# Kernel optimization log

Measured on AMD Instinct MI355X. Metric: run time of the kernel, lower is better.

## Reference

```python
import jax, jax.numpy as jnp
import numpy as np

N_EMBD = 768
N_HEAD = 12
HEAD_DIM = N_EMBD // N_HEAD  # 64


def setup_inputs() -> dict:
    key = jax.random.key(0)
    k1, k2, k3 = jax.random.split(key, 3)
    B, S = 4, 2048
    x = jax.random.normal(k1, (B, S, N_EMBD), dtype=jnp.float32)
    W_attn = jax.random.normal(k2, (N_EMBD, 3 * N_EMBD), dtype=jnp.float32) * 0.02
    b_attn = jax.random.normal(k3, (3 * N_EMBD,), dtype=jnp.float32) * 0.02
    return {"x": x, "W_attn": W_attn, "b_attn": b_attn}


def reference(x, W_attn, b_attn):
    B, S, E = x.shape
    H, D = N_HEAD, HEAD_DIM
    # fused QKV projection (torch Linear: x @ W^T + b; here W_attn stored as [E, 3E])
    qkv = x @ W_attn + b_attn  # [B, S, 3E]
    q, k, v = jnp.split(qkv, 3, axis=-1)
    q = q.reshape(B, S, H, D)
    k = k.reshape(B, S, H, D)
    v = v.reshape(B, S, H, D)
    scale = 1.0 / np.sqrt(D).astype(np.float32)
    scores = jnp.einsum('bqhd,bkhd->bhqk', q, k) * scale  # [B, H, S, S]
    causal = jnp.tril(jnp.ones((S, S), dtype=bool))
    # ReLU attention nonlinearity (no softmax); masked entries -> 0
    att = jnp.where(causal, jnp.maximum(scores, 0.0), 0.0)
    y = jnp.einsum('bhqk,bkhd->bqhd', att, v)  # [B, S, H, D]
    return y.reshape(B, S, E)
```

## Files before the change

### kernel.cpp

```cpp
#include <hip/hip_runtime.h>

typedef __attribute__((ext_vector_type(8))) short short8;
typedef __attribute__((ext_vector_type(4))) float floatx4;
typedef __attribute__((ext_vector_type(4))) unsigned int uint4v;

#define S_LEN 2048
#define NH 12
#define HD 64
#define EMB 768
#define E3 2304

#define MF(a, b, c) __builtin_amdgcn_mfma_f32_16x16x32_bf16(a, b, c, 0, 0, 0)

__device__ __forceinline__ unsigned short f2bf(float f) {
    unsigned int u = __builtin_bit_cast(unsigned int, f);
    u += 0x7FFFu + ((u >> 16) & 1u);
    return (unsigned short)(u >> 16);
}

__device__ __forceinline__ unsigned int pack2bf(float a, float b) {
#if __has_builtin(__builtin_amdgcn_cvt_pk_bf16_f32)
    typedef __attribute__((ext_vector_type(2))) short short2v;
    short2v r = __builtin_amdgcn_cvt_pk_bf16_f32(a, b);
    return __builtin_bit_cast(unsigned int, r);
#else
    return (unsigned int)f2bf(a) | ((unsigned int)f2bf(b) << 16);
#endif
}

__device__ __forceinline__ void pl32_swap(unsigned int& x, unsigned int& y) {
#if __has_builtin(__builtin_amdgcn_permlane32_swap)
    typedef __attribute__((ext_vector_type(2))) unsigned int uint2v_;
    uint2v_ r = __builtin_amdgcn_permlane32_swap(x, y, false, false);
    x = r[0]; y = r[1];
#else
    asm("v_permlane32_swap_b32 %0, %1" : "+v"(x), "+v"(y));
#endif
}
__device__ __forceinline__ void pl16_swap(unsigned int& x, unsigned int& y) {
#if __has_builtin(__builtin_amdgcn_permlane16_swap)
    typedef __attribute__((ext_vector_type(2))) unsigned int uint2v_;
    uint2v_ r = __builtin_amdgcn_permlane16_swap(x, y, false, false);
    x = r[0]; y = r[1];
#else
    asm("v_permlane16_swap_b32 %0, %1" : "+v"(x), "+v"(y));
#endif
}

__device__ __forceinline__ void gl_lds16(const void* g, void* l) {
    __builtin_amdgcn_global_load_lds(
        (const __attribute__((address_space(1))) unsigned int*)g,
        (__attribute__((address_space(3))) unsigned int*)l, 16, 0, 0);
}

__global__ __launch_bounds__(256) void conv_fused(const float* __restrict__ x,
                                                  ushort* __restrict__ xb,
                                                  const float* __restrict__ W,
                                                  ushort* __restrict__ Wt) {
    int tid = threadIdx.x;
    if (blockIdx.x < 6144) {
        int i = (blockIdx.x * 256 + tid) * 4;
        float4 f = *(const float4*)(x + i);
        ushort4 o;
        o.x = f2bf(f.x); o.y = f2bf(f.y); o.z = f2bf(f.z); o.w = f2bf(f.w);
        *(ushort4*)(xb + i) = o;
    } else {
        __shared__ float tile[32][33];
        int b2 = blockIdx.x - 6144;
        int n0 = (b2 % 72) * 32, k0 = (b2 / 72) * 32;
        int tx = tid & 31, ty = tid >> 5;
        for (int i = 0; i < 4; i++)
            tile[ty + i * 8][tx] = W[(size_t)(k0 + ty + i * 8) * E3 + n0 + tx];
        __syncthreads();
        for (int i = 0; i < 4; i++)
            Wt[(size_t)(n0 + ty + i * 8) * EMB + k0 + tx] = f2bf(tile[tx][ty + i * 8]);
    }
}

__global__ __launch_bounds__(512, 1) void qkv_gemm(const ushort* __restrict__ Xb,
                                                   const ushort* __restrict__ Wt,
                                                   const float* __restrict__ bias,
                                                   ushort* __restrict__ QKb,
                                                   ushort* __restrict__ Vt) {
    extern __shared__ char ldsb[];
    const int tid  = threadIdx.x;
    const int w = tid >> 6, lane = tid & 63;
    const int l15 = lane & 15, quad = lane >> 4;
    const int r8 = lane >> 3, cc = lane & 7;
    const int wm = w >> 1, wn = w & 1;
    const int m0 = blockIdx.x * 256, n0 = blockIdx.y * 128;

    floatx4 acc[4][4] = {};

    const char* agp = (const char*)Xb + (size_t)(m0 + w * 32 + r8) * 1536 + (cc ^ r8) * 16;
    const char* bgp = (const char*)Wt + (size_t)(n0 + w * 16 + r8) * 1536 + (cc ^ r8) * 16;
    const int adstB = w * 4096;
    const int bdstB = 32768 + w * 2048;

    const int aroB = (wm * 64 + l15) * 128;
    const int broB = 32768 + (wn * 64 + l15) * 128;
    const int swz0 = ((quad) ^ (l15 & 7)) * 16;
    const int swz1 = ((4 + quad) ^ (l15 & 7)) * 16;

    for (int i = 0; i < 4; i++) gl_lds16(agp + i * 12288, ldsb + adstB + i * 1024);
    for (int i = 0; i < 2; i++) gl_lds16(bgp + i * 12288, ldsb + bdstB + i * 1024);
    for (int i = 0; i < 4; i++) gl_lds16(agp + 128 + i * 12288, ldsb + 49152 + adstB + i * 1024);
    for (int i = 0; i < 2; i++) gl_lds16(bgp + 128 + i * 12288, ldsb + 49152 + bdstB + i * 1024);

#pragma unroll
    for (int t = 0; t < 12; ++t) {
        if (t < 11) asm volatile("s_waitcnt vmcnt(6)" ::: "memory");
        else        asm volatile("s_waitcnt vmcnt(0)" ::: "memory");
        __builtin_amdgcn_s_barrier();
        __builtin_amdgcn_sched_barrier(0);

        const char* base = ldsb + (t % 3) * 49152;
        char* sdst = ldsb + ((t + 2) % 3) * 49152;
        const int koff = (t + 2) * 128;
        const bool st = (t < 10);

        short8 af0, af1, bf0, bf1, bf2, bf3;

        af0 = *(const short8*)(base + aroB + 0 * 2048 + swz0);
        af1 = *(const short8*)(base + aroB + 1 * 2048 + swz0);
        bf0 = *(const short8*)(base + broB + 0 * 2048 + swz0);
        bf1 = *(const short8*)(base + broB + 1 * 2048 + swz0);
        bf2 = *(const short8*)(base + broB + 2 * 2048 + swz0);
        bf3 = *(const short8*)(base + broB + 3 * 2048 + swz0);
        if (st) { gl_lds16(agp + koff,         sdst + adstB);
                  gl_lds16(agp + koff + 12288, sdst + adstB + 1024); }
        __builtin_amdgcn_s_setprio(1);
        acc[0][0] = MF(af0, bf0, acc[0][0]); acc[0][1] = MF(af0, bf1, acc[0][1]);
        acc[0][2] = MF(af0, bf2, acc[0][2]); acc[0][3] = MF(af0, bf3, acc[0][3]);
        acc[1][0] = MF(af1, bf0, acc[1][0]); acc[1][1] = MF(af1, bf1, acc[1][1]);
        acc[1][2] = MF(af1, bf2, acc[1][2]); acc[1][3] = MF(af1, bf3, acc[1][3]);
        __builtin_amdgcn_s_setprio(0);
        __builtin_amdgcn_s_barrier();

        af0 = *(const short8*)(base + aroB + 2 * 2048 + swz0);
        af1 = *(const short8*)(base + aroB + 3 * 2048 + swz0);
        if (st) { gl_lds16(agp + koff + 2 * 12288, sdst + adstB + 2048);
                  gl_lds16(agp + koff + 3 * 12288, sdst + adstB + 3072); }
        __builtin_amdgcn_s_setprio(1);
        acc[2][0] = MF(af0, bf0, acc[2][0]); acc[2][1] = MF(af0, bf1, acc[2][1]);
        acc[2][2] = MF(af0, bf2, acc[2][2]); acc[2][3] = MF(af0, bf3, acc[2][3]);
        acc[3][0] = MF(af1, bf0, acc[3][0]); acc[3][1] = MF(af1, bf1, acc[3][1]);
        acc[3][2] = MF(af1, bf2, acc[3][2]); acc[3][3] = MF(af1, bf3, acc[3][3]);
        __builtin_amdgcn_s_setprio(0);
        __builtin_amdgcn_s_barrier();

        af0 = *(const short8*)(base + aroB + 0 * 2048 + swz1);
        af1 = *(const short8*)(base + aroB + 1 * 2048 + swz1);
        bf0 = *(const short8*)(base + broB + 0 * 2048 + swz1);
        bf1 = *(const short8*)(base + broB + 1 * 2048 + swz1);
        bf2 = *(const short8*)(base + broB + 2 * 2048 + swz1);
        bf3 = *(const short8*)(base + broB + 3 * 2048 + swz1);
        if (st) { gl_lds16(bgp + koff,         sdst + bdstB);
                  gl_lds16(bgp + koff + 12288, sdst + bdstB + 1024); }
        __builtin_amdgcn_s_setprio(1);
        acc[0][0] = MF(af0, bf0, acc[0][0]); acc[0][1] = MF(af0, bf1, acc[0][1]);
        acc[0][2] = MF(af0, bf2, acc[0][2]); acc[0][3] = MF(af0, bf3, acc[0][3]);
        acc[1][0] = MF(af1, bf0, acc[1][0]); acc[1][1] = MF(af1, bf1, acc[1][1]);
        acc[1][2] = MF(af1, bf2, acc[1][2]); acc[1][3] = MF(af1, bf3, acc[1][3]);
        __builtin_amdgcn_s_setprio(0);
        __builtin_amdgcn_s_barrier();

        af0 = *(const short8*)(base + aroB + 2 * 2048 + swz1);
        af1 = *(const short8*)(base + aroB + 3 * 2048 + swz1);
        __builtin_amdgcn_s_setprio(1);
        acc[2][0] = MF(af0, bf0, acc[2][0]); acc[2][1] = MF(af0, bf1, acc[2][1]);
        acc[2][2] = MF(af0, bf2, acc[2][2]); acc[2][3] = MF(af0, bf3, acc[2][3]);
        acc[3][0] = MF(af1, bf0, acc[3][0]); acc[3][1] = MF(af1, bf1, acc[3][1]);
        acc[3][2] = MF(af1, bf2, acc[3][2]); acc[3][3] = MF(af1, bf3, acc[3][3]);
        __builtin_amdgcn_s_setprio(0);
    }

    __syncthreads();
    ushort* epi = (ushort*)ldsb;
    int seg = n0 >= 1536 ? 2 : (n0 >= 768 ? 1 : 0);
    if (seg < 2) {
        float scale = (seg == 0) ? 0.125f : 1.0f;
        for (int ni = 0; ni < 4; ni++) {
            int nl = wn * 64 + ni * 16 + l15;
            float bv = bias[n0 + nl];
            for (int mi = 0; mi < 4; mi++)
                for (int r = 0; r < 4; r++) {
                    int ml = wm * 64 + mi * 16 + quad * 4 + r;
                    epi[ml * 132 + nl] = f2bf((acc[mi][ni][r] + bv) * scale);
                }
        }
        __syncthreads();
        int row = tid >> 1, h2 = tid & 1;
        size_t gm = (size_t)(m0 + row);
        for (int i = 0; i < 8; i++) {
            uint4 v = *(const uint4*)&epi[row * 132 + h2 * 64 + i * 8];
            *(uint4*)&QKb[gm * 1536 + n0 + h2 * 64 + i * 8] = v;
        }
    } else {
        for (int ni = 0; ni < 4; ni++) {
            int nl = wn * 64 + ni * 16 + l15;
            float bv = bias[n0 + nl];
            for (int mi = 0; mi < 4; mi++) {
                int ml = wm * 64 + mi * 16 + quad * 4;
                ushort4 p4;
                p4.x = f2bf(acc[mi][ni][0] + bv);
                p4.y = f2bf(acc[mi][ni][1] + bv);
                p4.z = f2bf(acc[mi][ni][2] + bv);
                p4.w = f2bf(acc[mi][ni][3] + bv);
                *(ushort4*)&epi[nl * 264 + ml] = p4;
            }
        }
        __syncthreads();
        int row = tid >> 2, q4 = tid & 3;
        int nn = n0 + row - 1536;
        int hh = nn >> 6, d = nn & 63;
        int bb = m0 >> 11, s0 = m0 & 2047;
        for (int i = 0; i < 8; i++) {
            uint4 v = *(const uint4*)&epi[row * 264 + q4 * 64 + i * 8];
            *(uint4*)&Vt[((size_t)(bb * NH + hh) * HD + d) * S_LEN + s0 + q4 * 64 + i * 8] = v;
        }
    }
}

__global__ __launch_bounds__(128, 2) void attn(const ushort* __restrict__ QKb,
                                               const ushort* __restrict__ Vt,
                                               float* __restrict__ out) {
    __shared__ ushort lds[16384];
    char* ldsb = (char*)lds;
    int tid = threadIdx.x;
    int w = tid >> 6, lane = tid & 63;
    int l15 = lane & 15, quad = lane >> 4;
    int r8 = lane >> 3, cc = lane & 7;

    int kfo[2];
    for (int ch = 0; ch < 2; ch++)
        kfo[ch] = l15 * 128 + ((ch * 4 + quad) ^ (l15 & 7)) * 16;
    int vfo[2];
    for (int T = 0; T < 2; T++)
        vfo[T] = 16384 + l15 * 128 + ((T * 4 + quad) ^ (l15 & 7)) * 16;
    int rhs[2] = { w * 32 + l15, w * 32 + 16 + l15 };
    int kgo = (w * 32 + r8) * 3072 + (cc ^ r8) * 16;
    int vgo[4];
    for (int i = 0; i < 4; i++)
        vgo[i] = (w * 32 + i * 8 + r8) * 4096 + (cc ^ r8) * 16;
    int kst = (w * 32) * 128;
    int vst = 16384 + (w * 32) * 128;

    int b = blockIdx.x;
    int qs = 31 - b / 48, bh = b % 48;
    int bg = bh / NH, h = bh % NH;

    const char* kg = (const char*)(QKb + (size_t)bg * S_LEN * 1536 + 768 + h * 64) + kgo;
    const char* vgb = (const char*)(Vt + (size_t)bh * HD * S_LEN);

    auto prefetch = [&](int st, int dstP) {
        const char* kbase = kg + (size_t)st * 196608;
        const char* vbase = vgb + st * 128;
        for (int i = 0; i < 4; i++)
            gl_lds16(kbase + i * 24576, ldsb + dstP * 8192 + kst + i * 1024);
        for (int i = 0; i < 4; i++)
            gl_lds16(vbase + vgo[i], ldsb + dstP * 8192 + vst + i * 1024);
    };

    const ushort* Qcol = QKb + (size_t)bg * S_LEN * 1536 + h * 64;
    short8 qf[2][2];
    for (int nq = 0; nq < 2; nq++)
        for (int ch = 0; ch < 2; ch++)
            qf[nq][ch] = *(const short8*)(Qcol +
                (size_t)(qs * 64 + w * 32 + nq * 16 + l15) * 1536 + ch * 32 + quad * 8);

    floatx4 acco[2][4] = {};
    int p = 0;
    prefetch(0, 0);
    int nst = qs + 1;
    for (int st = 0; st < nst; st++) {
        __syncthreads();
        if (st + 1 < nst) prefetch(st + 1, p ^ 1);

        bool diag = (st == qs);
        const char* kb = ldsb + p * 8192;

        floatx4 stc[4][2] = {};
        for (int ch = 0; ch < 2; ch++) {
            short8 kf[4];
            for (int mk = 0; mk < 4; mk++)
                kf[mk] = *(const short8*)(kb + kfo[ch] + mk * 2048);
            for (int mk = 0; mk < 4; mk++)
                for (int nq = 0; nq < 2; nq++)
                    stc[mk][nq] = __builtin_amdgcn_mfma_f32_16x16x32_bf16(
                        kf[mk], qf[nq][ch], stc[mk][nq], 0, 0, 0);
        }

        unsigned int pk[4][2][2];
        for (int mk = 0; mk < 4; mk++) {
            for (int nq = 0; nq < 2; nq++) {
                float e[4];
                for (int r = 0; r < 4; r++)
                    e[r] = fmaxf(stc[mk][nq][r], 0.0f);
                if (diag) {
                    int kl = mk * 16 + quad * 4;
                    for (int r = 0; r < 4; r++)
                        if (kl + r > rhs[nq]) e[r] = 0.0f;
                }
                pk[mk][nq][0] = pack2bf(e[0], e[1]);
                pk[mk][nq][1] = pack2bf(e[2], e[3]);
            }
        }

        for (int pr = 0; pr < 2; pr++) {
            short8 vf[4];
            for (int ni = 0; ni < 4; ni++)
                vf[ni] = *(const short8*)(kb + vfo[pr] + ni * 2048);
            for (int mi = 0; mi < 2; mi++) {
                unsigned int a0 = pk[2 * pr][mi][0], a1 = pk[2 * pr][mi][1];
                unsigned int b0 = pk[2 * pr + 1][mi][0], b1 = pk[2 * pr + 1][mi][1];
                pl32_swap(a0, b0);  pl32_swap(a1, b1);
                pl16_swap(a0, b0);  pl16_swap(a1, b1);
                short8 af = __builtin_bit_cast(short8, (uint4v){a0, a1, b0, b1});
                for (int ni = 0; ni < 4; ni++)
                    acco[mi][ni] = __builtin_amdgcn_mfma_f32_16x16x32_bf16(
                        af, vf[ni], acco[mi][ni], 0, 0, 0);
            }
        }
        p ^= 1;
    }

    for (int mi = 0; mi < 2; mi++) {
        for (int ni = 0; ni < 4; ni++) {
            int d = ni * 16 + l15;
            for (int r = 0; r < 4; r++) {
                int s = qs * 64 + w * 32 + mi * 16 + quad * 4 + r;
                out[((size_t)bg * S_LEN + s) * EMB + h * 64 + d] = acco[mi][ni][r];
            }
        }
    }
}

extern "C" void kernel_launch(void* const* d_in, const int* in_sizes, int n_in,
                              void* d_out, int out_size, void* d_ws, size_t ws_size,
                              hipStream_t stream) {
    const float* x    = (const float*)d_in[0];
    const float* W    = (const float*)d_in[1];
    const float* bias = (const float*)d_in[2];
    float* out = (float*)d_out;

    char* ws = (char*)d_ws;
    const size_t SZ_X  = (size_t)8192 * EMB * 2;
    const size_t SZ_W  = (size_t)E3 * EMB * 2;
    const size_t SZ_QK = (size_t)8192 * 1536 * 2;
    ushort* Xb  = (ushort*)(ws);
    ushort* Wt  = (ushort*)(ws + SZ_X);
    ushort* QKb = (ushort*)(ws + SZ_X + SZ_W);
    ushort* Vt  = (ushort*)(ws + SZ_X + SZ_W + SZ_QK);

    static bool attr_done = false;
    if (!attr_done) {
        hipFuncSetAttribute((const void*)qkv_gemm,
                            hipFuncAttributeMaxDynamicSharedMemorySize, 147456);
        attr_done = true;
    }

    conv_fused<<<dim3(6144 + 1728), dim3(256), 0, stream>>>(x, Xb, W, Wt);
    qkv_gemm<<<dim3(32, 18), dim3(512), 147456, stream>>>(Xb, Wt, bias, QKb, Vt);
    attn<<<dim3(1536), dim3(128), 0, stream>>>(QKb, Vt, out);
}
```

Measured before the change: 186.0 us.

## Restructure causal attention into balanced 128-row query tiles with triple-buffered prefetch

The attention kernel now uses 256-thread blocks, each covering a 128-row query tile. Causal work is balanced by pairing a long tile with a short tile in one block, so the grid drops to 480 blocks with roughly even load. K/V loads become a three-stage LDS ring with explicit vmcnt waits and raw barriers, and MFMA sections are wrapped in s_setprio. This targets load imbalance, idle tail blocks and pipeline stalls, at the cost of more LDS per block, more complex indexing and a skip of fully masked diagonal work.

```diff
diff --git a/kernel.cpp b/kernel.cpp
--- a/kernel.cpp
+++ b/kernel.cpp
@@ -222,10 +222,10 @@
     }
 }
 
-__global__ __launch_bounds__(128, 2) void attn(const ushort* __restrict__ QKb,
+__global__ __launch_bounds__(256, 3) void attn(const ushort* __restrict__ QKb,
                                                const ushort* __restrict__ Vt,
                                                float* __restrict__ out) {
-    __shared__ ushort lds[16384];
+    __shared__ ushort lds[24576];
     char* ldsb = (char*)lds;
     int tid = threadIdx.x;
     int w = tid >> 6, lane = tid & 63;
@@ -236,103 +236,132 @@
     for (int ch = 0; ch < 2; ch++)
         kfo[ch] = l15 * 128 + ((ch * 4 + quad) ^ (l15 & 7)) * 16;
     int vfo[2];
-    for (int T = 0; T < 2; T++)
-        vfo[T] = 16384 + l15 * 128 + ((T * 4 + quad) ^ (l15 & 7)) * 16;
+    for (int pr = 0; pr < 2; pr++)
+        vfo[pr] = 8192 + l15 * 128 + ((pr * 4 + quad) ^ (l15 & 7)) * 16;
     int rhs[2] = { w * 32 + l15, w * 32 + 16 + l15 };
-    int kgo = (w * 32 + r8) * 3072 + (cc ^ r8) * 16;
-    int vgo[4];
-    for (int i = 0; i < 4; i++)
-        vgo[i] = (w * 32 + i * 8 + r8) * 4096 + (cc ^ r8) * 16;
-    int kst = (w * 32) * 128;
-    int vst = 16384 + (w * 32) * 128;
+    int kgo = (w * 16 + r8) * 3072 + (cc ^ r8) * 16;
+    int vgo = (w * 16 + r8) * 4096 + (cc ^ r8) * 16;
+    int kst = (w * 16) * 128;
+    int vst = 8192 + (w * 16) * 128;
 
     int b = blockIdx.x;
-    int qs = 31 - b / 48, bh = b % 48;
+    int g = b & 7, idx = b >> 3;
+    int role = idx / 6;
+    int bh = g * 6 + (idx % 6);
+    int nit, qt0, qt1;
+    if (role < 4) { nit = 1; qt0 = 15 - role; qt1 = 0; }
+    else          { nit = 2; qt0 = 15 - role; qt1 = role - 4; }
     int bg = bh / NH, h = bh % NH;
+    int n0 = 2 * qt0 + 2;
+    int ntot = n0 + (nit == 2 ? 2 * qt1 + 2 : 0);
 
     const char* kg = (const char*)(QKb + (size_t)bg * S_LEN * 1536 + 768 + h * 64) + kgo;
-    const char* vgb = (const char*)(Vt + (size_t)bh * HD * S_LEN);
-
-    auto prefetch = [&](int st, int dstP) {
-        const char* kbase = kg + (size_t)st * 196608;
-        const char* vbase = vgb + st * 128;
-        for (int i = 0; i < 4; i++)
-            gl_lds16(kbase + i * 24576, ldsb + dstP * 8192 + kst + i * 1024);
-        for (int i = 0; i < 4; i++)
-            gl_lds16(vbase + vgo[i], ldsb + dstP * 8192 + vst + i * 1024);
+    const char* vg = (const char*)(Vt + (size_t)bh * HD * S_LEN) + vgo;
+
+    const ushort* Qcol = QKb + (size_t)bg * S_LEN * 1536 + h * 64;
+    short8 qf[2][2][2];
+    for (int it = 0; it < 2; it++) {
+        int qt = it ? qt1 : qt0;
+        for (int nq = 0; nq < 2; nq++)
+            for (int ch = 0; ch < 2; ch++)
+                qf[it][nq][ch] = *(const short8*)(Qcol +
+                    (size_t)(qt * 128 + w * 32 + nq * 16 + l15) * 1536 + ch * 32 + quad * 8);
+    }
+
+    auto pf = [&](int j) {
+        int st = (j < n0) ? j : j - n0;
+        char* rb = ldsb + (j % 3) * 16384;
+        const char* ks = kg + (size_t)st * 196608;
+        const char* vs = vg + st * 128;
+        gl_lds16(ks,         rb + kst);
+        gl_lds16(ks + 24576, rb + kst + 1024);
+        gl_lds16(vs,         rb + vst);
+        gl_lds16(vs + 32768, rb + vst + 1024);
     };
 
-    const ushort* Qcol = QKb + (size_t)bg * S_LEN * 1536 + h * 64;
-    short8 qf[2][2];
-    for (int nq = 0; nq < 2; nq++)
-        for (int ch = 0; ch < 2; ch++)
-            qf[nq][ch] = *(const short8*)(Qcol +
-                (size_t)(qs * 64 + w * 32 + nq * 16 + l15) * 1536 + ch * 32 + quad * 8);
-
+    pf(0); pf(1);
     floatx4 acco[2][4] = {};
-    int p = 0;
-    prefetch(0, 0);
-    int nst = qs + 1;
-    for (int st = 0; st < nst; st++) {
-        __syncthreads();
-        if (st + 1 < nst) prefetch(st + 1, p ^ 1);
-
-        bool diag = (st == qs);
-        const char* kb = ldsb + p * 8192;
-
-        floatx4 stc[4][2] = {};
-        for (int ch = 0; ch < 2; ch++) {
-            short8 kf[4];
+    for (int i = 0; i < ntot; i++) {
+        if (i + 1 < ntot) asm volatile("s_waitcnt vmcnt(4)" ::: "memory");
+        else              asm volatile("s_waitcnt vmcnt(0)" ::: "memory");
+        __builtin_amdgcn_s_barrier();
+        __builtin_amdgcn_sched_barrier(0);
+        if (i + 2 < ntot) pf(i + 2);
+
+        int it = (i < n0) ? 0 : 1;
+        int st = it ? i - n0 : i;
+        int qt = it ? qt1 : qt0;
+        int dstage = st - 2 * qt;
+        const char* rb = ldsb + (i % 3) * 16384;
+
+        if (!(dstage == 1 && w < 2)) {
+            floatx4 stc[4][2] = {};
+            __builtin_amdgcn_s_setprio(1);
+            for (int ch = 0; ch < 2; ch++) {
+                short8 kf[4];
+                for (int mk = 0; mk < 4; mk++)
+                    kf[mk] = *(const short8*)(rb + kfo[ch] + mk * 2048);
+                for (int mk = 0; mk < 4; mk++)
+                    for (int nq = 0; nq < 2; nq++)
+                        stc[mk][nq] = MF(kf[mk], qf[it][nq][ch], stc[mk][nq]);
+            }
+            __builtin_amdgcn_s_setprio(0);
+
+            unsigned int pk[4][2][2];
             for (int mk = 0; mk < 4; mk++)
-                kf[mk] = *(const short8*)(kb + kfo[ch] + mk * 2048);
-            for (int mk = 0; mk < 4; mk++)
-                for (int nq = 0; nq < 2; nq++)
-                    stc[mk][nq] = __builtin_amdgcn_mfma_f32_16x16x32_bf16(
-                        kf[mk], qf[nq][ch], stc[mk][nq], 0, 0, 0);
-        }
-
-        unsigned int pk[4][2][2];
-        for (int mk = 0; mk < 4; mk++) {
-            for (int nq = 0; nq < 2; nq++) {
-                float e[4];
-                for (int r = 0; r < 4; r++)
-                    e[r] = fmaxf(stc[mk][nq][r], 0.0f);
-                if (diag) {
-                    int kl = mk * 16 + quad * 4;
+                for (int nq = 0; nq < 2; nq++) {
+                    float e[4];
                     for (int r = 0; r < 4; r++)
-                        if (kl + r > rhs[nq]) e[r] = 0.0f;
-                }
-                pk[mk][nq][0] = pack2bf(e[0], e[1]);
-                pk[mk][nq][1] = pack2bf(e[2], e[3]);
+                        e[r] = fmaxf(stc[mk][nq][r], 0.0f);
+                    if (dstage >= 0) {
+                        int kl = mk * 16 + quad * 4;
+                        int lim = rhs[nq] - dstage * 64;
+                        for (int r = 0; r < 4; r++)
+                            if (kl + r > lim) e[r] = 0.0f;
+                    }
+                    pk[mk][nq][0] = pack2bf(e[0], e[1]);
+                    pk[mk][nq][1] = pack2bf(e[2], e[3]);
+                }
+
+            __builtin_amdgcn_s_setprio(1);
+            for (int pr = 0; pr < 2; pr++) {
+                short8 vf[4];
+                for (int ni = 0; ni < 4; ni++)
+                    vf[ni] = *(const short8*)(rb + vfo[pr] + ni * 2048);
+                for (int mi = 0; mi < 2; mi++) {
+                    unsigned int a0 = pk[2 * pr][mi][0], a1 = pk[2 * pr][mi][1];
+                    unsigned int b0 = pk[2 * pr + 1][mi][0], b1 = pk[2 * pr + 1][mi][1];
+                    pl32_swap(a0, b0);  pl32_swap(a1, b1);
+                    pl16_swap(a0, b0);  pl16_swap(a1, b1);
+                    short8 af = __builtin_bit_cast(short8, (uint4v){a0, a1, b0, b1});
+                    for (int ni = 0; ni < 4; ni++)
+                        acco[mi][ni] = MF(af, vf[ni], acco[mi][ni]);
+                }
             }
-        }
-
-        for (int pr = 0; pr < 2; pr++) {
-            short8 vf[4];
-            for (int ni = 0; ni < 4; ni++)
-                vf[ni] = *(const short8*)(kb + vfo[pr] + ni * 2048);
-            for (int mi = 0; mi < 2; mi++) {
-                unsigned int a0 = pk[2 * pr][mi][0], a1 = pk[2 * pr][mi][1];
-                unsigned int b0 = pk[2 * pr + 1][mi][0], b1 = pk[2 * pr + 1][mi][1];
-                pl32_swap(a0, b0);  pl32_swap(a1, b1);
-                pl16_swap(a0, b0);  pl16_swap(a1, b1);
-                short8 af = __builtin_bit_cast(short8, (uint4v){a0, a1, b0, b1});
-                for (int ni = 0; ni < 4; ni++)
-                    acco[mi][ni] = __builtin_amdgcn_mfma_f32_16x16x32_bf16(
-                        af, vf[ni], acco[mi][ni], 0, 0, 0);
+            __builtin_amdgcn_s_setprio(0);
+        }
+
+        if (i == n0 - 1) {
+            for (int mi = 0; mi < 2; mi++)
+                for (int ni = 0; ni < 4; ni++) {
+                    int d = ni * 16 + l15;
+                    for (int r = 0; r < 4; r++) {
+                        int s = qt0 * 128 + w * 32 + mi * 16 + quad * 4 + r;
+                        out[((size_t)bg * S_LEN + s) * EMB + h * 64 + d] = acco[mi][ni][r];
+                    }
+                    acco[mi][ni] = (floatx4){0.f, 0.f, 0.f, 0.f};
+                }
+        }
+    }
+    if (nit == 2) {
+        for (int mi = 0; mi < 2; mi++)
+            for (int ni = 0; ni < 4; ni++) {
+                int d = ni * 16 + l15;
+                for (int r = 0; r < 4; r++) {
+                    int s = qt1 * 128 + w * 32 + mi * 16 + quad * 4 + r;
+                    out[((size_t)bg * S_LEN + s) * EMB + h * 64 + d] = acco[mi][ni][r];
+                }
             }
-        }
-        p ^= 1;
-    }
-
-    for (int mi = 0; mi < 2; mi++) {
-        for (int ni = 0; ni < 4; ni++) {
-            int d = ni * 16 + l15;
-            for (int r = 0; r < 4; r++) {
-                int s = qs * 64 + w * 32 + mi * 16 + quad * 4 + r;
-                out[((size_t)bg * S_LEN + s) * EMB + h * 64 + d] = acco[mi][ni][r];
-            }
-        }
     }
 }
 
@@ -362,5 +391,5 @@
 
     conv_fused<<<dim3(6144 + 1728), dim3(256), 0, stream>>>(x, Xb, W, Wt);
     qkv_gemm<<<dim3(32, 18), dim3(512), 147456, stream>>>(Xb, Wt, bias, QKb, Vt);
-    attn<<<dim3(1536), dim3(128), 0, stream>>>(QKb, Vt, out);
-}
+    attn<<<dim3(480), dim3(256), 0, stream>>>(QKb, Vt, out);
+}
```

New measurement: 178.5 us. 1.04x faster.
